# Kernel optimization log

Hardware: AMD Instinct MI355X
Metric: run time of the kernel (lower is better)

The kernel has to match this reference:

```python
import jax, jax.numpy as jnp
import numpy as np

ALPHA = 0.2        # LeakyReLU slope
NEG_BIG = -9e15    # mask fill value from the original module


def setup_inputs() -> dict:
    key = jax.random.key(0)
    k1, k2, k3, k4 = jax.random.split(key, 4)
    N, F_IN, F_OUT = 8192, 256, 128
    h = jax.random.normal(k1, (N, F_IN), dtype=jnp.float32)
    adj = jax.random.randint(k2, (N, N), 0, 2, dtype=jnp.int32)
    W = jax.random.normal(k3, (F_IN, F_OUT), dtype=jnp.float32) * (1.0 / np.sqrt(F_IN))
    a = jax.random.normal(k4, (2 * F_OUT, 1), dtype=jnp.float32) * (1.0 / np.sqrt(2 * F_OUT))
    return {"h": h, "adj": adj, "W": W, "a": a}


def reference(h, adj, W, a):
    f_out = W.shape[1]
    Wh = h @ W                                   # [N, F_out]
    Wh1 = Wh @ a[:f_out, :]                      # [N, 1]
    Wh2 = Wh @ a[f_out:, :]                      # [N, 1]
    e = Wh1 + Wh2.T                              # [N, N] broadcast-add
    e = jnp.where(e > 0, e, ALPHA * e)           # LeakyReLU
    e = jnp.where(adj > 0, e, NEG_BIG)           # adjacency mask
    attention = jax.nn.softmax(e, axis=-1)       # row softmax
    # dropout rate = 0.0 -> identity
    h_prime = attention @ Wh                     # [N, F_out]
    return jax.nn.elu(h_prime)
```

## Files before the change

### kernel.cpp

```cpp
#include <hip/hip_runtime.h>

#define NV 8192
#define FIN 256
#define FOUT 128
#define SPLITS 8
#define PANEL 1024

typedef __bf16 bf16_t;
typedef __attribute__((ext_vector_type(8))) __bf16 bf16x8;
typedef __attribute__((ext_vector_type(4))) float f32x4;
typedef __attribute__((ext_vector_type(4))) int i32x4;

__global__ __launch_bounds__(256) void wh_kernel(
    const float* __restrict__ h, const float* __restrict__ W,
    const float* __restrict__ a,
    bf16_t* __restrict__ Wg, float* __restrict__ Wh1, float* __restrict__ Wh2)
{
  __shared__ float As[64][34];
  __shared__ float Bs[64][128];
  __shared__ float Cs[32][129];
  __shared__ float red1[32][16];
  __shared__ float red2[32][16];
  const int t  = threadIdx.x;
  const int i0 = blockIdx.x * 32;
  const int c  = t & 15;
  const int r  = t >> 4;
  float acc0[8], acc1[8];
  #pragma unroll
  for (int j = 0; j < 8; j++) { acc0[j] = 0.f; acc1[j] = 0.f; }

  for (int k0 = 0; k0 < FIN; k0 += 64) {
    {
      const int ia = t >> 3;
      const int ka = (t & 7) * 8;
      const float* src = h + (size_t)(i0 + ia) * FIN + k0 + ka;
      float4 v0 = *(const float4*)src;
      float4 v1 = *(const float4*)(src + 4);
      As[ka+0][ia]=v0.x; As[ka+1][ia]=v0.y; As[ka+2][ia]=v0.z; As[ka+3][ia]=v0.w;
      As[ka+4][ia]=v1.x; As[ka+5][ia]=v1.y; As[ka+6][ia]=v1.z; As[ka+7][ia]=v1.w;
    }
    {
      const int kb = t >> 2;
      const int cb = (t & 3) * 32;
      const float4* src = (const float4*)(W + (size_t)(k0 + kb) * FOUT + cb);
      float4* dst = (float4*)&Bs[kb][cb];
      #pragma unroll
      for (int q = 0; q < 8; q++) dst[q] = src[q];
    }
    __syncthreads();
    #pragma unroll 4
    for (int k = 0; k < 64; k++) {
      float2 av = *(const float2*)&As[k][r*2];
      float b[8];
      *(float4*)&b[0] = *(const float4*)&Bs[k][c*8];
      *(float4*)&b[4] = *(const float4*)&Bs[k][c*8+4];
      #pragma unroll
      for (int j = 0; j < 8; j++) {
        acc0[j] = fmaf(av.x, b[j], acc0[j]);
        acc1[j] = fmaf(av.y, b[j], acc1[j]);
      }
    }
    __syncthreads();
  }

  float p1a = 0.f, p2a = 0.f, p1b = 0.f, p2b = 0.f;
  #pragma unroll
  for (int j = 0; j < 8; j++) {
    Cs[r*2][c*8+j]   = acc0[j];
    Cs[r*2+1][c*8+j] = acc1[j];
    float w1 = a[c*8+j];
    float w2 = a[FOUT + c*8+j];
    p1a = fmaf(acc0[j], w1, p1a); p2a = fmaf(acc0[j], w2, p2a);
    p1b = fmaf(acc1[j], w1, p1b); p2b = fmaf(acc1[j], w2, p2b);
  }
  red1[r*2][c]   = p1a; red2[r*2][c]   = p2a;
  red1[r*2+1][c] = p1b; red2[r*2+1][c] = p2b;
  __syncthreads();
  if (t < 32) {
    float s = 0.f;
    #pragma unroll
    for (int q = 0; q < 16; q++) s += red1[t][q];
    Wh1[i0 + t] = s;
  } else if (t < 64) {
    float s = 0.f;
    #pragma unroll
    for (int q = 0; q < 16; q++) s += red2[t-32][q];
    Wh2[i0 + t - 32] = s;
  }
  {
    const int f = t & 127, half = t >> 7;
    const int fb = f >> 4, f15 = f & 15;
    union { bf16_t b[8]; uint4 v; } p0, p1;
    #pragma unroll
    for (int q = 0; q < 8; q++) {
      p0.b[q] = (bf16_t)Cs[half*16 + q][f];
      p1.b[q] = (bf16_t)Cs[half*16 + 8 + q][f];
    }
    size_t base = (size_t)(i0 >> 5) * 4096 + (size_t)fb * 512
                + (size_t)(2*half) * 128 + (size_t)f15 * 8;
    *(uint4*)(Wg + base)       = p0.v;
    *(uint4*)(Wg + base + 128) = p1.v;
  }
}

#define LOADC(buf, jc) do {                                                   \
    buf[0] = __builtin_nontemporal_load((const i32x4*)(rowp + (jc)));         \
    buf[1] = __builtin_nontemporal_load((const i32x4*)(rowp + (jc) + 4));     \
    buf[2] = __builtin_nontemporal_load((const i32x4*)(rowp + (jc) + 32));    \
    buf[3] = __builtin_nontemporal_load((const i32x4*)(rowp + (jc) + 32 + 4));\
  } while (0)

#define PCOMP(buf, jc, s, af) do {                                            \
    const i32x4 aa = buf[(s)*2], ab = buf[(s)*2+1];                           \
    const int am[8] = {aa.x,aa.y,aa.z,aa.w, ab.x,ab.y,ab.z,ab.w};             \
    float4 wA = *(const float4*)&Wh2s[(jc) + (s)*32 + kh8];                   \
    float4 wB = *(const float4*)&Wh2s[(jc) + (s)*32 + kh8 + 4];               \
    const float wm[8] = {wA.x,wA.y,wA.z,wA.w, wB.x,wB.y,wB.z,wB.w};           \
    _Pragma("unroll")                                                         \
    for (int q = 0; q < 8; q++) {                                             \
      float e = wh1 + wm[q];                                                  \
      e = fmaxf(e, 0.2f * e);                             \
      float p = (am[q] > 0) ? __expf(e) : 0.0f;               \
      den_t += p;                                                             \
      af[q] = (bf16_t)p;                                                      \
    } } while (0)

#define BODY(BUF, JC, NJC) do {                                               \
    bf16x8 af0, af1;                                                          \
    PCOMP(BUF, (JC), 0, af0);                                                 \
    PCOMP(BUF, (JC), 1, af1);                                                 \
    const bf16_t* bb0 = Wg + (size_t)((j0 + (JC)) >> 5) * 4096 + lane8;       \
    const bf16_t* bb1 = Wg + (size_t)((j0 + (JC) + 32) >> 5) * 4096 + lane8;  \
    bf16x8 b0[8], b1[8];                                                      \
    _Pragma("unroll")                                                         \
    for (int fb = 0; fb < 8; fb++) {                                          \
      b0[fb] = *(const bf16x8*)(bb0 + fb * 512);                              \
      b1[fb] = *(const bf16x8*)(bb1 + fb * 512);                              \
    }                                                                         \
    __builtin_amdgcn_sched_barrier(0);                                        \
    LOADC(BUF, (NJC));                                                        \
    __builtin_amdgcn_sched_barrier(0);                                        \
    _Pragma("unroll")                                                         \
    for (int fb = 0; fb < 8; fb++) {                                          \
      acc[fb] = __builtin_amdgcn_mfma_f32_16x16x32_bf16(af0, b0[fb],          \
                                                        acc[fb], 0, 0, 0);    \
      acc[fb] = __builtin_amdgcn_mfma_f32_16x16x32_bf16(af1, b1[fb],          \
                                                        acc[fb], 0, 0, 0);    \
    } } while (0)

__global__ __launch_bounds__(256, 3) void attn_kernel(
    const int* __restrict__ adj, const bf16_t* __restrict__ Wg,
    const float* __restrict__ Wh1v, const float* __restrict__ Wh2v,
    float* __restrict__ nump, float* __restrict__ denp)
{
  __shared__ float Wh2s[PANEL];
  const int t     = threadIdx.x;
  const int lane  = t & 63;
  const int w     = t >> 6;
  const int f15   = lane & 15;
  const int kh    = lane >> 4;
  const int kh8   = kh * 8;
  const int lane8 = lane * 8;
  const int rb    = blockIdx.x >> 3;
  const int split = blockIdx.x & 7;
  const int i0    = rb * 64;
  const int j0    = split * PANEL;
  const int row   = i0 + w * 16 + f15;
  const float wh1 = Wh1v[row];
  const int* rowp = adj + (size_t)row * NV + j0 + kh8;

  *(float4*)&Wh2s[t * 4] = *(const float4*)(Wh2v + j0 + t * 4);
  __syncthreads();

  f32x4 acc[8] = {};
  float den_t = 0.f;
  i32x4 c0[4], c1[4];

  LOADC(c0, 0);
  LOADC(c1, 64);
  #pragma unroll 1
  for (int jc = 0; jc < PANEL; jc += 128) {
    BODY(c0, jc,      (jc + 128) & (PANEL - 1));
    BODY(c1, jc + 64, (jc + 192) & (PANEL - 1));
  }

  den_t += __shfl_xor(den_t, 16, 64);
  den_t += __shfl_xor(den_t, 32, 64);
  if (lane < 16) denp[(size_t)split * NV + i0 + w * 16 + lane] = den_t;

  float* base = nump + ((size_t)split * NV + i0 + w * 16) * FOUT;
  #pragma unroll
  for (int fb = 0; fb < 8; fb++) {
    #pragma unroll
    for (int reg = 0; reg < 4; reg++) {
      const int crow = kh * 4 + reg;
      base[(size_t)crow * FOUT + fb * 16 + f15] = acc[fb][reg];
    }
  }
}

__global__ __launch_bounds__(256) void finalize_kernel(
    const float* __restrict__ nump, const float* __restrict__ denp,
    float* __restrict__ out)
{
  const int gid = blockIdx.x * 256 + threadIdx.x;
  const int i  = gid >> 5;
  const int f0 = (gid & 31) * 4;
  float den = 0.f;
  #pragma unroll
  for (int s = 0; s < SPLITS; s++) den += denp[(size_t)s * NV + i];
  float4 sv = make_float4(0.f, 0.f, 0.f, 0.f);
  #pragma unroll
  for (int s = 0; s < SPLITS; s++) {
    float4 v = *(const float4*)&nump[((size_t)s * NV + i) * FOUT + f0];
    sv.x += v.x; sv.y += v.y; sv.z += v.z; sv.w += v.w;
  }
  const float inv = 1.0f / den;
  float4 r;
  r.x = sv.x * inv; r.y = sv.y * inv; r.z = sv.z * inv; r.w = sv.w * inv;
  r.x = r.x > 0.f ? r.x : __expf(r.x) - 1.0f;
  r.y = r.y > 0.f ? r.y : __expf(r.y) - 1.0f;
  r.z = r.z > 0.f ? r.z : __expf(r.z) - 1.0f;
  r.w = r.w > 0.f ? r.w : __expf(r.w) - 1.0f;
  *(float4*)&out[(size_t)i * FOUT + f0] = r;
}

extern "C" void kernel_launch(void* const* d_in, const int* in_sizes, int n_in,
                              void* d_out, int out_size, void* d_ws, size_t ws_size,
                              hipStream_t stream) {
  const float* h  = (const float*)d_in[0];
  const int*  adj = (const int*)d_in[1];
  const float* W  = (const float*)d_in[2];
  const float* a  = (const float*)d_in[3];
  float* out = (float*)d_out;
  char* ws = (char*)d_ws;
  bf16_t* Wg  = (bf16_t*)ws;
  float* Wh1  = (float*)(ws + 2097152);
  float* Wh2  = (float*)(ws + 2097152 + 32768);
  float* denp = (float*)(ws + 2097152 + 65536);
  float* nump = (float*)(ws + 2097152 + 65536 + 262144);

  wh_kernel<<<256, 256, 0, stream>>>(h, W, a, Wg, Wh1, Wh2);
  attn_kernel<<<1024, 256, 0, stream>>>(adj, Wg, Wh1, Wh2, nump, denp);
  finalize_kernel<<<1024, 256, 0, stream>>>(nump, denp, out);
}
```

Measured before the change: 439.6 us.

## Software-pipeline Wh B-operand loads one chunk ahead in attention kernel

Restructures the attention main loop into 32-column chunks. The bf16 Wh B fragments for the next chunk are double-buffered in registers, and adjacency loads are prefetched two chunks ahead, so the loads overlap with the current chunk's MFMAs. Previously the B fragments were loaded and consumed in the same step, which exposed their latency. The change keeps the same register footprint (two 8-entry B buffers) but issues smaller, more frequent load batches.

```diff
diff --git a/kernel.cpp b/kernel.cpp
--- a/kernel.cpp
+++ b/kernel.cpp
@@ -5,6 +5,7 @@
 #define FOUT 128
 #define SPLITS 8
 #define PANEL 1024
+#define NCHUNK 32
 
 typedef __bf16 bf16_t;
 typedef __attribute__((ext_vector_type(8))) __bf16 bf16x8;
@@ -103,18 +104,22 @@
   }
 }
 
-#define LOADC(buf, jc) do {                                                   \
-    buf[0] = __builtin_nontemporal_load((const i32x4*)(rowp + (jc)));         \
-    buf[1] = __builtin_nontemporal_load((const i32x4*)(rowp + (jc) + 4));     \
-    buf[2] = __builtin_nontemporal_load((const i32x4*)(rowp + (jc) + 32));    \
-    buf[3] = __builtin_nontemporal_load((const i32x4*)(rowp + (jc) + 32 + 4));\
-  } while (0)
-
-#define PCOMP(buf, jc, s, af) do {                                            \
-    const i32x4 aa = buf[(s)*2], ab = buf[(s)*2+1];                           \
+#define LOADA(A, c) do {                                                      \
+    A[0] = __builtin_nontemporal_load((const i32x4*)(rowp + (c) * 32));       \
+    A[1] = __builtin_nontemporal_load((const i32x4*)(rowp + (c) * 32 + 4));   \
+  } while (0)
+
+#define LOADB(B, c) do {                                                      \
+    _Pragma("unroll")                                                         \
+    for (int fb = 0; fb < 8; fb++)                                            \
+      B[fb] = *(const bf16x8*)(panelp + (size_t)(c) * 4096 + fb * 512);       \
+  } while (0)
+
+#define PCOMP(af, A, c) do {                                                  \
+    const i32x4 aa = A[0], ab = A[1];                                         \
     const int am[8] = {aa.x,aa.y,aa.z,aa.w, ab.x,ab.y,ab.z,ab.w};             \
-    float4 wA = *(const float4*)&Wh2s[(jc) + (s)*32 + kh8];                   \
-    float4 wB = *(const float4*)&Wh2s[(jc) + (s)*32 + kh8 + 4];               \
+    float4 wA = *(const float4*)&Wh2s[(c) * 32 + kh8];                        \
+    float4 wB = *(const float4*)&Wh2s[(c) * 32 + kh8 + 4];                    \
     const float wm[8] = {wA.x,wA.y,wA.z,wA.w, wB.x,wB.y,wB.z,wB.w};           \
     _Pragma("unroll")                                                         \
     for (int q = 0; q < 8; q++) {                                             \
@@ -125,28 +130,22 @@
       af[q] = (bf16_t)p;                                                      \
     } } while (0)
 
-#define BODY(BUF, JC, NJC) do {                                               \
-    bf16x8 af0, af1;                                                          \
-    PCOMP(BUF, (JC), 0, af0);                                                 \
-    PCOMP(BUF, (JC), 1, af1);                                                 \
-    const bf16_t* bb0 = Wg + (size_t)((j0 + (JC)) >> 5) * 4096 + lane8;       \
-    const bf16_t* bb1 = Wg + (size_t)((j0 + (JC) + 32) >> 5) * 4096 + lane8;  \
-    bf16x8 b0[8], b1[8];                                                      \
+#define MFMA8(af, B) do {                                                     \
     _Pragma("unroll")                                                         \
-    for (int fb = 0; fb < 8; fb++) {                                          \
-      b0[fb] = *(const bf16x8*)(bb0 + fb * 512);                              \
-      b1[fb] = *(const bf16x8*)(bb1 + fb * 512);                              \
-    }                                                                         \
+    for (int fb = 0; fb < 8; fb++)                                            \
+      acc[fb] = __builtin_amdgcn_mfma_f32_16x16x32_bf16(af, B[fb],            \
+                                                        acc[fb], 0, 0, 0);    \
+  } while (0)
+
+#define BODY(A, Bcur, Bnxt, c) do {                                           \
+    bf16x8 af;                                                                \
+    PCOMP(af, A, (c));                                                        \
     __builtin_amdgcn_sched_barrier(0);                                        \
-    LOADC(BUF, (NJC));                                                        \
+    LOADB(Bnxt, ((c) + 1) & (NCHUNK - 1));                                    \
+    LOADA(A,    ((c) + 2) & (NCHUNK - 1));                                    \
     __builtin_amdgcn_sched_barrier(0);                                        \
-    _Pragma("unroll")                                                         \
-    for (int fb = 0; fb < 8; fb++) {                                          \
-      acc[fb] = __builtin_amdgcn_mfma_f32_16x16x32_bf16(af0, b0[fb],          \
-                                                        acc[fb], 0, 0, 0);    \
-      acc[fb] = __builtin_amdgcn_mfma_f32_16x16x32_bf16(af1, b1[fb],          \
-                                                        acc[fb], 0, 0, 0);    \
-    } } while (0)
+    MFMA8(af, Bcur);                                                          \
+  } while (0)
 
 __global__ __launch_bounds__(256, 3) void attn_kernel(
     const int* __restrict__ adj, const bf16_t* __restrict__ Wg,
@@ -160,7 +159,6 @@
   const int f15   = lane & 15;
   const int kh    = lane >> 4;
   const int kh8   = kh * 8;
-  const int lane8 = lane * 8;
   const int rb    = blockIdx.x >> 3;
   const int split = blockIdx.x & 7;
   const int i0    = rb * 64;
@@ -168,20 +166,23 @@
   const int row   = i0 + w * 16 + f15;
   const float wh1 = Wh1v[row];
   const int* rowp = adj + (size_t)row * NV + j0 + kh8;
+  const bf16_t* panelp = Wg + (size_t)(j0 >> 5) * 4096 + lane * 8;
 
   *(float4*)&Wh2s[t * 4] = *(const float4*)(Wh2v + j0 + t * 4);
   __syncthreads();
 
   f32x4 acc[8] = {};
   float den_t = 0.f;
-  i32x4 c0[4], c1[4];
-
-  LOADC(c0, 0);
-  LOADC(c1, 64);
+  i32x4 a0[2], a1[2];
+  bf16x8 bb0[8], bb1[8];
+
+  LOADB(bb0, 0);
+  LOADA(a0, 0);
+  LOADA(a1, 1);
   #pragma unroll 1
-  for (int jc = 0; jc < PANEL; jc += 128) {
-    BODY(c0, jc,      (jc + 128) & (PANEL - 1));
-    BODY(c1, jc + 64, (jc + 192) & (PANEL - 1));
+  for (int c = 0; c < NCHUNK; c += 2) {
+    BODY(a0, bb0, bb1, c);
+    BODY(a1, bb1, bb0, c + 1);
   }
 
   den_t += __shfl_xor(den_t, 16, 64);
```

After: 429.5 us. -2.3%, faster.
